# Kernel tuning notes

Hardware: AMD Instinct MI355X
Metric: run time of the kernel (lower is better)

Reference implementation:

```python
import jax, jax.numpy as jnp
import numpy as np

B, S, H, NH = 2, 2048, 128, 8  # batch, seq, num_hidden (= per-head dim), num_heads
LN_EPS = 1e-5


def _ln(x, g, b):
    m = jnp.mean(x, axis=-1, keepdims=True)
    v = jnp.var(x, axis=-1, keepdims=True)
    return (x - m) / jnp.sqrt(v + LN_EPS) * g + b


def setup_inputs() -> dict:
    key = jax.random.key(0)
    ks = jax.random.split(key, 18)
    sc = 0.02
    d = {}
    d["x"] = jax.random.normal(ks[0], (B, S, H), jnp.float32)
    # per-head full-dim projections, stacked over heads: [NH, H, H] (in->out layout)
    d["Wq"] = jax.random.normal(ks[1], (NH, H, H), jnp.float32) * sc
    d["bq"] = jax.random.normal(ks[2], (NH, H), jnp.float32) * sc
    d["Wk"] = jax.random.normal(ks[3], (NH, H, H), jnp.float32) * sc
    d["bk"] = jax.random.normal(ks[4], (NH, H), jnp.float32) * sc
    d["Wv"] = jax.random.normal(ks[5], (NH, H, H), jnp.float32) * sc
    d["bv"] = jax.random.normal(ks[6], (NH, H), jnp.float32) * sc
    d["Wo"] = jax.random.normal(ks[7], (NH * H, H), jnp.float32) * sc
    d["bo"] = jax.random.normal(ks[8], (H,), jnp.float32) * sc
    # conv1x1 FFN == pointwise linears: [H, 2H] and [2H, H]
    d["W1"] = jax.random.normal(ks[9], (H, 2 * H), jnp.float32) * sc
    d["b1"] = jax.random.normal(ks[10], (2 * H,), jnp.float32) * sc
    d["W2"] = jax.random.normal(ks[11], (2 * H, H), jnp.float32) * sc
    d["b2"] = jax.random.normal(ks[12], (H,), jnp.float32) * sc
    d["g1"] = jnp.ones((H,), jnp.float32)
    d["beta1"] = jnp.zeros((H,), jnp.float32)
    d["g2"] = jnp.ones((H,), jnp.float32)
    d["beta2"] = jnp.zeros((H,), jnp.float32)
    return d


def reference(x, Wq, bq, Wk, bk, Wv, bv, Wo, bo, W1, b1, W2, b2, g1, beta1, g2, beta2):
    # Multi-head attention: each head uses the FULL embed dim (faithful to source).
    Q = jnp.einsum('bsd,hde->bhse', x, Wq) + bq[None, :, None, :]
    K = jnp.einsum('bsd,hde->bhse', x, Wk) + bk[None, :, None, :]
    V = jnp.einsum('bsd,hde->bhse', x, Wv) + bv[None, :, None, :]
    scores = jnp.einsum('bhse,bhte->bhst', Q, K) / jnp.sqrt(jnp.float32(H))
    A = jax.nn.softmax(scores, axis=-1)          # [B, NH, S, S]
    o = jnp.einsum('bhst,bhte->bhse', A, V)      # [B, NH, S, H]
    o = o.transpose(0, 2, 1, 3).reshape(x.shape[0], x.shape[1], NH * H)  # concat heads
    y = o @ Wo + bo                               # W_O projection
    y = _ln(y, g1, beta1)                         # norm1 (no residual around attn, per source)
    f = jax.nn.relu(jax.nn.relu(y @ W1 + b1) @ W2 + b2)  # conv1x1 -> relu -> conv1x1 -> relu
    y = _ln(y + f, g2, beta2)                     # residual + norm2
    return y
```

## Files before the change

### kernel.cpp

```cpp
#include <hip/hip_runtime.h>
#include <math.h>

#define Bq  2
#define Sq  2048
#define Hq  128
#define NHq 8

typedef __attribute__((ext_vector_type(8))) short bf16x8;
typedef __attribute__((ext_vector_type(4))) float f32x4;
typedef __attribute__((ext_vector_type(16))) float f32x16;
typedef __attribute__((ext_vector_type(4))) unsigned short ushort4_t;
typedef __attribute__((ext_vector_type(4))) unsigned int uint4v;
typedef __attribute__((ext_vector_type(2))) unsigned long long u64x2;
typedef unsigned short ushort_t;
typedef unsigned int uint_t;
typedef unsigned long long u64;

__device__ inline ushort_t f2bf(float f) {
    union { float f; uint_t u; } c; c.f = f;
    uint_t u = c.u + 0x7FFFu + ((c.u >> 16) & 1u);
    return (ushort_t)(u >> 16);
}
__device__ inline float bf2f(ushort_t u) {
    union { uint_t u; float f; } c; c.u = ((uint_t)u) << 16;
    return c.f;
}

__device__ inline uint_t cvtpk_bf16(float lo, float hi) {
    uint_t r;
    asm("v_cvt_pk_bf16_f32 %0, %1, %2" : "=v"(r) : "v"(lo), "v"(hi));
    return r;
}
__device__ inline void pswap32(uint_t &a, uint_t &b) {
    asm("v_permlane32_swap_b32 %0, %1" : "+v"(a), "+v"(b));
}

#define GLOAD16(gsrc, ldst) \
    __builtin_amdgcn_global_load_lds( \
        (const __attribute__((address_space(1))) unsigned int*)(const void*)(gsrc), \
        (__attribute__((address_space(3))) unsigned int*)(ldst), 16, 0, 0)

__global__ __launch_bounds__(256) void tw_kernel(
    const float* __restrict__ Wq, const float* __restrict__ Wk, const float* __restrict__ Wv,
    const float* __restrict__ Wo, const float* __restrict__ W1, const float* __restrict__ W2,
    ushort_t* __restrict__ Wt_all, ushort_t* __restrict__ Wot,
    ushort_t* __restrict__ W1t, ushort_t* __restrict__ W2t)
{
    const int z = blockIdx.y;
    const float* src; ushort_t* dst; int R, C;
    if (z < 24) { const int h = z & 7;
        src = (z < 8 ? Wq : z < 16 ? Wk : Wv) + h * 16384;
        dst = Wt_all + z * 16384; R = 128; C = 128;
    } else if (z == 24) { src = Wo; dst = Wot; R = 1024; C = 128; }
    else if (z == 25)   { src = W1; dst = W1t; R = 128;  C = 256; }
    else                { src = W2; dst = W2t; R = 256;  C = 128; }

    const int tpc = C >> 5;
    if ((int)blockIdx.x >= (R >> 5) * tpc) return;
    const int r0 = (blockIdx.x / tpc) << 5;
    const int c0 = (blockIdx.x % tpc) << 5;

    __shared__ float ls[32][33];
    const int t = threadIdx.x;
    const int lr = t >> 5, lc = t & 31;
    #pragma unroll
    for (int i = 0; i < 4; ++i)
        ls[lr + i * 8][lc] = src[(size_t)(r0 + lr + i * 8) * C + c0 + lc];
    __syncthreads();
    const int wc = t >> 3, wr0 = (t & 7) << 2;
    ushort4_t o4;
    o4[0] = f2bf(ls[wr0 + 0][wc]); o4[1] = f2bf(ls[wr0 + 1][wc]);
    o4[2] = f2bf(ls[wr0 + 2][wc]); o4[3] = f2bf(ls[wr0 + 3][wc]);
    *(ushort4_t*)&dst[(size_t)(c0 + wc) * R + r0 + wr0] = o4;
}

__global__ __launch_bounds__(256) void qkv_gemm(
    const float* __restrict__ x, const ushort_t* __restrict__ Wt_all,
    const float* __restrict__ bq, const float* __restrict__ bk, const float* __restrict__ bv,
    ushort_t* __restrict__ Qb, ushort_t* __restrict__ Kb, ushort_t* __restrict__ Vb)
{
    __shared__ ushort_t As[64 * 128];
    __shared__ ushort_t Bs[128 * 128];
    const int tid = threadIdx.x;
    const int w = tid >> 6, l = tid & 63, lg = l >> 4, ln = l & 15;
    const int m0 = blockIdx.x << 6;
    const int z  = blockIdx.y;

    #pragma unroll
    for (int i = 0; i < 4; ++i) {
        const int c = tid + i * 256;
        const int row = c >> 4, j = c & 15;
        const float* xp = x + (size_t)(m0 + row) * 128 + j * 8;
        const float4 a = *(const float4*)xp;
        const float4 b = *(const float4*)(xp + 4);
        bf16x8 v;
        v[0]=f2bf(a.x); v[1]=f2bf(a.y); v[2]=f2bf(a.z); v[3]=f2bf(a.w);
        v[4]=f2bf(b.x); v[5]=f2bf(b.y); v[6]=f2bf(b.z); v[7]=f2bf(b.w);
        *(bf16x8*)&As[row * 128 + ((j ^ (row & 15)) << 3)] = v;
    }
    const ushort_t* Wz = Wt_all + (size_t)z * 16384;
    #pragma unroll
    for (int i = 0; i < 8; ++i) {
        const int seg = w * 8 + i;
        const int row = seg * 4 + (l >> 4);
        const int j = (l & 15) ^ (row & 15);
        GLOAD16(Wz + row * 128 + j * 8, &Bs[seg * 512]);
    }
    __syncthreads();

    bf16x8 af[4];
    #pragma unroll
    for (int kc = 0; kc < 4; ++kc)
        af[kc] = *(const bf16x8*)&As[(w * 16 + ln) * 128 + (((kc * 4 + lg) ^ ln) << 3)];

    f32x4 acc[8];
    #pragma unroll
    for (int nt = 0; nt < 8; ++nt) acc[nt] = (f32x4){0.f,0.f,0.f,0.f};
    #pragma unroll
    for (int nt = 0; nt < 8; ++nt)
        #pragma unroll
        for (int kc = 0; kc < 4; ++kc) {
            const bf16x8 bn = *(const bf16x8*)&Bs[(nt * 16 + ln) * 128 + (((kc * 4 + lg) ^ ln) << 3)];
            acc[nt] = __builtin_amdgcn_mfma_f32_16x16x32_bf16(af[kc], bn, acc[nt], 0, 0, 0);
        }

    const float* bias = (z < 8 ? bq : z < 16 ? bk : bv) + (z & 7) * 128;
    ushort_t* outp = (z < 8 ? Qb : z < 16 ? Kb : Vb);
    const float scale = z < 8 ? 0.08838834764831845f : 1.0f;
    const int h = z & 7;
    #pragma unroll
    for (int nt = 0; nt < 8; ++nt) {
        const float bb = bias[nt * 16 + ln];
        #pragma unroll
        for (int j2 = 0; j2 < 4; ++j2) {
            const int r = m0 + w * 16 + lg * 4 + j2;
            const int b = r >> 11, s = r & 2047;
            outp[((size_t)((b << 3) + h) * 2048 + s) * 128 + nt * 16 + ln] =
                f2bf((acc[nt][j2] + bb) * scale);
        }
    }
}

__global__ __launch_bounds__(256, 2) void attn_kernel(
    const ushort_t* __restrict__ Q, const ushort_t* __restrict__ K,
    const ushort_t* __restrict__ V, ushort_t* __restrict__ Opart,
    float2* __restrict__ ml)
{
    __shared__ ushort_t sh[32768];
    ushort_t* Vt = sh + 16384;

    const int tid = threadIdx.x;
    const int w = tid >> 6, l = tid & 63;
    const int ln5 = l & 31, h5 = l >> 5;

    const int id  = blockIdx.x;
    const int id2 = (id & 7) * 64 + (id >> 3);
    const int s   = id2 >> 8;
    const int bh  = (id2 >> 4) & 15;
    const int q0  = (id2 & 15) << 7;
    const int kv0 = s << 10;

    const size_t base = (size_t)bh * Sq * Hq;
    const ushort_t* Qp = Q + base;
    const ushort_t* Kp = K + base + (size_t)kv0 * Hq;
    const ushort_t* Vp = V + base + (size_t)kv0 * Hq;

    bf16x8 qf[8];
    {
        const ushort_t* qrow = Qp + (size_t)(q0 + w * 32 + ln5) * Hq;
        #pragma unroll
        for (int kc = 0; kc < 8; ++kc)
            qf[kc] = *(const bf16x8*)(qrow + kc * 16 + h5 * 8);
    }

    const int kv2 = (tid & 31) * 2;
    const int d8  = (tid >> 5) * 8;

    f32x16 po[4];
    #pragma unroll
    for (int dt = 0; dt < 4; ++dt)
        #pragma unroll
        for (int r = 0; r < 16; ++r) po[dt][r] = 0.f;
    float m_ = -1e30f, l_ = 0.f;

    #pragma unroll
    for (int i = 0; i < 4; ++i) {
        const int seg = w * 4 + i;
        const int row = seg * 4 + (l >> 4);
        const int j = (l & 15) ^ (row & 15);
        GLOAD16(Kp + (size_t)row * Hq + j * 8, &sh[seg * 512]);
    }
    bf16x8 va0 = *(const bf16x8*)(Vp + (size_t)kv2 * Hq + d8);
    bf16x8 va1 = *(const bf16x8*)(Vp + (size_t)(kv2 + 1) * Hq + d8);
    bf16x8 vb0 = *(const bf16x8*)(Vp + (size_t)kv2 * Hq + d8 + 64);
    bf16x8 vb1 = *(const bf16x8*)(Vp + (size_t)(kv2 + 1) * Hq + d8 + 64);
    __syncthreads();
    #pragma unroll
    for (int jj = 0; jj < 8; ++jj) {
        const int r1 = d8 + jj, r2 = d8 + 64 + jj;
        *(uint_t*)&Vt[r1 * 128 + ((((kv2 >> 3) ^ (r1 & 15))) << 3) + (kv2 & 7)] =
            (uint_t)(ushort_t)va0[jj] | ((uint_t)(ushort_t)va1[jj] << 16);
        *(uint_t*)&Vt[r2 * 128 + ((((kv2 >> 3) ^ (r2 & 15))) << 3) + (kv2 & 7)] =
            (uint_t)(ushort_t)vb0[jj] | ((uint_t)(ushort_t)vb1[jj] << 16);
    }
    __syncthreads();

    const int NT = 1024 / 64;
    for (int t = 0; t < NT; ++t) {
        const int buf = t & 1;
        const ushort_t* Ksb = sh + buf * 8192;

        f32x16 st[2];
        #pragma unroll
        for (int mt = 0; mt < 2; ++mt)
            #pragma unroll
            for (int r = 0; r < 16; ++r) st[mt][r] = 0.f;

        __builtin_amdgcn_s_setprio(1);
        #pragma unroll
        for (int kc = 0; kc < 8; ++kc) {
            #pragma unroll
            for (int mt = 0; mt < 2; ++mt) {
                const int row = mt * 32 + ln5;
                const int slot = (kc * 2 + h5) ^ (row & 15);
                const bf16x8 ka = *(const bf16x8*)&Ksb[row * 128 + (slot << 3)];
                st[mt] = __builtin_amdgcn_mfma_f32_32x32x16_bf16(ka, qf[kc], st[mt], 0, 0, 0);
            }
        }
        __builtin_amdgcn_s_setprio(0);

        if (t + 1 < NT) {
            const int k0n = (t + 1) * 64;
            #pragma unroll
            for (int i = 0; i < 4; ++i) {
                const int seg = w * 4 + i;
                const int row = seg * 4 + (l >> 4);
                const int j = (l & 15) ^ (row & 15);
                GLOAD16(Kp + (size_t)(k0n + row) * Hq + j * 8, &sh[(buf ^ 1) * 8192 + seg * 512]);
            }
            va0 = *(const bf16x8*)(Vp + (size_t)(k0n + kv2) * Hq + d8);
            va1 = *(const bf16x8*)(Vp + (size_t)(k0n + kv2 + 1) * Hq + d8);
            vb0 = *(const bf16x8*)(Vp + (size_t)(k0n + kv2) * Hq + d8 + 64);
            vb1 = *(const bf16x8*)(Vp + (size_t)(k0n + kv2 + 1) * Hq + d8 + 64);
        }

        float mxv[16];
        #pragma unroll
        for (int r = 0; r < 16; ++r) mxv[r] = fmaxf(st[0][r], st[1][r]);
        #pragma unroll
        for (int sd = 8; sd >= 1; sd >>= 1)
            #pragma unroll
            for (int i = 0; i < sd; ++i) mxv[i] = fmaxf(mxv[i], mxv[i + sd]);
        float mx = mxv[0];
        mx = fmaxf(mx, __shfl_xor(mx, 32));

        const bool anyup = __any(mx > m_ + 8.0f);
        float sc = 1.0f;
        if (anyup) {
            const float mn = fmaxf(m_, mx);
            sc = __expf(m_ - mn);
            m_ = mn;
        }

        float pe[32];
        #pragma unroll
        for (int mt = 0; mt < 2; ++mt)
            #pragma unroll
            for (int r = 0; r < 16; ++r)
                pe[mt * 16 + r] = __expf(st[mt][r] - m_);

        float sv[16];
        #pragma unroll
        for (int r = 0; r < 16; ++r) sv[r] = pe[r] + pe[16 + r];
        #pragma unroll
        for (int sd = 8; sd >= 1; sd >>= 1)
            #pragma unroll
            for (int i = 0; i < sd; ++i) sv[i] += sv[i + sd];
        float rs = sv[0];
        rs += __shfl_xor(rs, 32);
        l_ = l_ * sc + rs;

        bf16x8 pb[4];
        #pragma unroll
        for (int ks = 0; ks < 4; ++ks) {
            const int o = (ks >> 1) * 16 + (ks & 1) * 8;
            uint_t wA = cvtpk_bf16(pe[o + 0], pe[o + 1]);
            uint_t wB = cvtpk_bf16(pe[o + 4], pe[o + 5]);
            pswap32(wA, wB);
            uint_t wC = cvtpk_bf16(pe[o + 2], pe[o + 3]);
            uint_t wD = cvtpk_bf16(pe[o + 6], pe[o + 7]);
            pswap32(wC, wD);
            uint4v wv; wv[0] = wA; wv[1] = wC; wv[2] = wB; wv[3] = wD;
            pb[ks] = __builtin_bit_cast(bf16x8, wv);
        }

        if (anyup) {
            #pragma unroll
            for (int dt = 0; dt < 4; ++dt)
                #pragma unroll
                for (int r = 0; r < 16; ++r) po[dt][r] *= sc;
        }

        __builtin_amdgcn_s_setprio(1);
        #pragma unroll
        for (int dt = 0; dt < 4; ++dt) {
            #pragma unroll
            for (int ks = 0; ks < 4; ++ks) {
                const int row = dt * 32 + ln5;
                const int slot = (ks * 2 + h5) ^ (row & 15);
                const bf16x8 va = *(const bf16x8*)&Vt[row * 128 + (slot << 3)];
                po[dt] = __builtin_amdgcn_mfma_f32_32x32x16_bf16(va, pb[ks], po[dt], 0, 0, 0);
            }
        }
        __builtin_amdgcn_s_setprio(0);

        __syncthreads();
        if (t + 1 < NT) {
            #pragma unroll
            for (int jj = 0; jj < 8; ++jj) {
                const int r1 = d8 + jj, r2 = d8 + 64 + jj;
                *(uint_t*)&Vt[r1 * 128 + ((((kv2 >> 3) ^ (r1 & 15))) << 3) + (kv2 & 7)] =
                    (uint_t)(ushort_t)va0[jj] | ((uint_t)(ushort_t)va1[jj] << 16);
                *(uint_t*)&Vt[r2 * 128 + ((((kv2 >> 3) ^ (r2 & 15))) << 3) + (kv2 & 7)] =
                    (uint_t)(ushort_t)vb0[jj] | ((uint_t)(ushort_t)vb1[jj] << 16);
            }
        }
        __syncthreads();
    }

    char* shb = (char*)sh;
    char* wb = shb + w * 8448;
    #pragma unroll
    for (int dt = 0; dt < 4; ++dt)
        #pragma unroll
        for (int r = 0; r < 16; r += 2) {
            const int d = dt * 32 + (r & 3) + 8 * (r >> 2) + 4 * h5;
            const uint_t pk = cvtpk_bf16(po[dt][r], po[dt][r + 1]);
            *(uint_t*)(wb + ln5 * 264 + d * 2) = pk;
        }
    const int rid0 = (s * 16 + bh) * 2048 + q0 + w * 32;
    #pragma unroll
    for (int rb = 0; rb < 8; ++rb) {
        const int qr = rb * 4 + (l >> 4);
        const char* rp = wb + qr * 264 + (l & 15) * 16;
        u64x2 vv;
        vv[0] = *(const u64*)rp;
        vv[1] = *(const u64*)(rp + 8);
        *(u64x2*)(Opart + (size_t)(rid0 + qr) * 128 + (l & 15) * 8) = vv;
    }
    if (h5 == 0)
        ml[rid0 + ln5] = make_float2(m_, l_);
}

__global__ __launch_bounds__(256) void merge_kernel(
    const ushort_t* __restrict__ Opart, const float2* __restrict__ ml,
    ushort_t* __restrict__ ob)
{
    const int t = threadIdx.x;
    const int rid = blockIdx.x * 16 + (t >> 4);
    const int d0 = (t & 15) * 8;
    const float2 ml1 = ml[rid];
    const float2 ml2 = ml[32768 + rid];
    const float M = fmaxf(ml1.x, ml2.x);
    const float w1 = __expf(ml1.x - M), w2 = __expf(ml2.x - M);
    const float inv = 1.0f / (w1 * ml1.y + w2 * ml2.y);
    const bf16x8 o1 = *(const bf16x8*)&Opart[(size_t)rid * 128 + d0];
    const bf16x8 o2 = *(const bf16x8*)&Opart[(size_t)(32768 + rid) * 128 + d0];
    const int bh = rid >> 11, q = rid & 2047;
    const int b = bh >> 3, h = bh & 7;
    ushort_t* dst = ob + (size_t)(b * 2048 + q) * 1024 + h * 128 + d0;
    ushort4_t lo, hi;
    #pragma unroll
    for (int j = 0; j < 8; ++j) {
        const float v = (w1 * bf2f((ushort_t)o1[j]) + w2 * bf2f((ushort_t)o2[j])) * inv;
        if (j < 4) lo[j] = f2bf(v); else hi[j - 4] = f2bf(v);
    }
    *(ushort4_t*)dst = lo;
    *(ushort4_t*)(dst + 4) = hi;
}

__global__ __launch_bounds__(256) void gemm32_kernel(
    const ushort_t* __restrict__ A, const ushort_t* __restrict__ Bt,
    const float* __restrict__ bias, float* __restrict__ Cf, ushort_t* __restrict__ Cb,
    int N, int K, int KS, int relu)
{
    __shared__ ushort_t As[32 * 128];
    __shared__ ushort_t Bs[128 * 128];
    const int tid = threadIdx.x;
    const int w = tid >> 6, l = tid & 63, lg = l >> 4, ln = l & 15;
    const int m0 = blockIdx.x << 5;
    const int n0 = blockIdx.y << 7;
    const int rw = (w & 1) * 16;
    const int cw = (w >> 1) * 4;

    f32x4 acc[4];
    #pragma unroll
    for (int nt = 0; nt < 4; ++nt) acc[nt] = (f32x4){0.f,0.f,0.f,0.f};

    for (int ks = 0; ks < KS; ++ks) {
        const int k0 = ks << 7;
        #pragma unroll
        for (int i = 0; i < 2; ++i) {
            const int seg = w * 2 + i;
            const int row = seg * 4 + (l >> 4);
            const int j = (l & 15) ^ (row & 15);
            GLOAD16(A + (size_t)(m0 + row) * K + k0 + j * 8, &As[seg * 512]);
        }
        #pragma unroll
        for (int i = 0; i < 8; ++i) {
            const int seg = w * 8 + i;
            const int row = seg * 4 + (l >> 4);
            const int j = (l & 15) ^ (row & 15);
            GLOAD16(Bt + (size_t)(n0 + row) * K + k0 + j * 8, &Bs[seg * 512]);
        }
        __syncthreads();

        bf16x8 af[4];
        #pragma unroll
        for (int kc = 0; kc < 4; ++kc)
            af[kc] = *(const bf16x8*)&As[(rw + ln) * 128 + (((kc * 4 + lg) ^ ln) << 3)];
        #pragma unroll
        for (int nt = 0; nt < 4; ++nt)
            #pragma unroll
            for (int kc = 0; kc < 4; ++kc) {
                const bf16x8 bn = *(const bf16x8*)&Bs[((cw + nt) * 16 + ln) * 128 + (((kc * 4 + lg) ^ ln) << 3)];
                acc[nt] = __builtin_amdgcn_mfma_f32_16x16x32_bf16(af[kc], bn, acc[nt], 0, 0, 0);
            }
        __syncthreads();
    }

    #pragma unroll
    for (int nt = 0; nt < 4; ++nt) {
        const int col = n0 + (cw + nt) * 16 + ln;
        const float bb = bias[col];
        #pragma unroll
        for (int j2 = 0; j2 < 4; ++j2) {
            const int r = m0 + rw + lg * 4 + j2;
            float v = acc[nt][j2] + bb;
            if (relu) v = fmaxf(v, 0.f);
            if (Cb) Cb[(size_t)r * N + col] = f2bf(v);
            else    Cf[(size_t)r * N + col] = v;
        }
    }
}

__global__ __launch_bounds__(256) void ln_kernel(
    const float* __restrict__ in, const float* __restrict__ res,
    const float* __restrict__ g, const float* __restrict__ bta,
    float* __restrict__ out, ushort_t* __restrict__ out_bf)
{
    const int lane = threadIdx.x & 63;
    const int row  = (blockIdx.x << 2) + (threadIdx.x >> 6);
    const int base = row * 128 + lane * 2;
    float2 v = *(const float2*)&in[base];
    if (res) {
        const float2 rv = *(const float2*)&res[base];
        v.x += rv.x; v.y += rv.y;
    }
    float s  = v.x + v.y;
    float sq = v.x * v.x + v.y * v.y;
    #pragma unroll
    for (int mm = 1; mm <= 32; mm <<= 1) {
        s  += __shfl_xor(s, mm);
        sq += __shfl_xor(sq, mm);
    }
    const float mean = s * (1.0f / 128.0f);
    const float var  = sq * (1.0f / 128.0f) - mean * mean;
    const float rstd = rsqrtf(var + 1e-5f);
    const float2 gv = *(const float2*)&g[lane * 2];
    const float2 bv = *(const float2*)&bta[lane * 2];
    float2 o;
    o.x = (v.x - mean) * rstd * gv.x + bv.x;
    o.y = (v.y - mean) * rstd * gv.y + bv.y;
    *(float2*)&out[base] = o;
    if (out_bf) {
        const uint_t pk = (uint_t)f2bf(o.x) | ((uint_t)f2bf(o.y) << 16);
        *(uint_t*)&out_bf[base] = pk;
    }
}

extern "C" void kernel_launch(void* const* d_in, const int* in_sizes, int n_in,
                              void* d_out, int out_size, void* d_ws, size_t ws_size,
                              hipStream_t stream)
{
    const float* x   = (const float*)d_in[0];
    const float* Wq  = (const float*)d_in[1];
    const float* bq  = (const float*)d_in[2];
    const float* Wk  = (const float*)d_in[3];
    const float* bk  = (const float*)d_in[4];
    const float* Wv  = (const float*)d_in[5];
    const float* bv  = (const float*)d_in[6];
    const float* Wo  = (const float*)d_in[7];
    const float* bo  = (const float*)d_in[8];
    const float* W1  = (const float*)d_in[9];
    const float* b1  = (const float*)d_in[10];
    const float* W2  = (const float*)d_in[11];
    const float* b2  = (const float*)d_in[12];
    const float* g1  = (const float*)d_in[13];
    const float* be1 = (const float*)d_in[14];
    const float* g2  = (const float*)d_in[15];
    const float* be2 = (const float*)d_in[16];
    (void)in_sizes; (void)n_in; (void)out_size; (void)ws_size;

    ushort_t* Wt_all = (ushort_t*)d_ws;
    ushort_t* Wot = Wt_all + 393216;
    ushort_t* W1t = Wot + 131072;
    ushort_t* W2t = W1t + 32768;
    ushort_t* Qb  = W2t + 32768;
    ushort_t* Kb  = Qb + 4194304;
    ushort_t* Vb  = Kb + 4194304;
    ushort_t* ob  = Vb + 4194304;
    ushort_t* yb  = ob + 4194304;
    ushort_t* h1  = yb + 524288;
    ushort_t* Opart = h1 + 1048576;
    float2*   ml    = (float2*)(Opart + 8388608);
    float* y0 = (float*)Opart;
    float* y  = y0 + 524288;
    float* f  = y  + 524288;

    tw_kernel   <<<dim3(128, 27), 256, 0, stream>>>(Wq, Wk, Wv, Wo, W1, W2, Wt_all, Wot, W1t, W2t);
    qkv_gemm    <<<dim3(64, 24),  256, 0, stream>>>(x, Wt_all, bq, bk, bv, Qb, Kb, Vb);
    attn_kernel <<<dim3(512),     256, 0, stream>>>(Qb, Kb, Vb, Opart, ml);
    merge_kernel<<<dim3(2048),    256, 0, stream>>>(Opart, ml, ob);
    gemm32_kernel<<<dim3(128, 1), 256, 0, stream>>>(ob, Wot, bo, y0, nullptr, 128, 1024, 8, 0);
    ln_kernel   <<<1024,          256, 0, stream>>>(y0, nullptr, g1, be1, y, yb);
    gemm32_kernel<<<dim3(128, 2), 256, 0, stream>>>(yb, W1t, b1, nullptr, h1, 256, 128, 1, 1);
    gemm32_kernel<<<dim3(128, 1), 256, 0, stream>>>(h1, W2t, b2, f, nullptr, 128, 256, 2, 1);
    ln_kernel   <<<1024,          256, 0, stream>>>(y, f, g2, be2, (float*)d_out, nullptr);
}
```

Baseline: 95.87 us.

## Split attention KV four ways, fuse merge into Wo+LN, fuse FFN2 with LN

Attention now splits the KV range into four 512-key chunks, launching 1024 blocks. Its shared memory shrinks through a packed Vt layout, so three blocks can fit per CU. The separate merge kernel, Wo GEMM and first layernorm become one kernel that combines the four partials while staging A tiles. The second FFN GEMM is fused with residual-add and layernorm, and x is pre-converted to bf16 in the weight-transpose kernel so qkv_gemm can use async global-to-LDS loads. This cuts launches and intermediate global traffic, at the cost of more partial-output traffic and a serial 8-step K loop with only 128 blocks in the fused Wo kernel.

```diff
diff --git a/kernel.cpp b/kernel.cpp
--- a/kernel.cpp
+++ b/kernel.cpp
@@ -43,10 +43,30 @@
 __global__ __launch_bounds__(256) void tw_kernel(
     const float* __restrict__ Wq, const float* __restrict__ Wk, const float* __restrict__ Wv,
     const float* __restrict__ Wo, const float* __restrict__ W1, const float* __restrict__ W2,
+    const float* __restrict__ x,
     ushort_t* __restrict__ Wt_all, ushort_t* __restrict__ Wot,
-    ushort_t* __restrict__ W1t, ushort_t* __restrict__ W2t)
+    ushort_t* __restrict__ W1t, ushort_t* __restrict__ W2t, ushort_t* __restrict__ xb)
 {
     const int z = blockIdx.y;
+    const int t = threadIdx.x;
+
+    if (z == 27) {
+        const int r0 = blockIdx.x << 5;
+        #pragma unroll
+        for (int i = 0; i < 2; ++i) {
+            const int c = t + i * 256;
+            const int row = r0 + (c >> 4), j = (c & 15) * 8;
+            const float* xp = x + (size_t)row * 128 + j;
+            const float4 a = *(const float4*)xp;
+            const float4 b = *(const float4*)(xp + 4);
+            bf16x8 v;
+            v[0]=f2bf(a.x); v[1]=f2bf(a.y); v[2]=f2bf(a.z); v[3]=f2bf(a.w);
+            v[4]=f2bf(b.x); v[5]=f2bf(b.y); v[6]=f2bf(b.z); v[7]=f2bf(b.w);
+            *(bf16x8*)&xb[(size_t)row * 128 + j] = v;
+        }
+        return;
+    }
+
     const float* src; ushort_t* dst; int R, C;
     if (z < 24) { const int h = z & 7;
         src = (z < 8 ? Wq : z < 16 ? Wk : Wv) + h * 16384;
@@ -61,7 +81,6 @@
     const int c0 = (blockIdx.x % tpc) << 5;
 
     __shared__ float ls[32][33];
-    const int t = threadIdx.x;
     const int lr = t >> 5, lc = t & 31;
     #pragma unroll
     for (int i = 0; i < 4; ++i)
@@ -75,7 +94,7 @@
 }
 
 __global__ __launch_bounds__(256) void qkv_gemm(
-    const float* __restrict__ x, const ushort_t* __restrict__ Wt_all,
+    const ushort_t* __restrict__ xb, const ushort_t* __restrict__ Wt_all,
     const float* __restrict__ bq, const float* __restrict__ bk, const float* __restrict__ bv,
     ushort_t* __restrict__ Qb, ushort_t* __restrict__ Kb, ushort_t* __restrict__ Vb)
 {
@@ -88,15 +107,10 @@
 
     #pragma unroll
     for (int i = 0; i < 4; ++i) {
-        const int c = tid + i * 256;
-        const int row = c >> 4, j = c & 15;
-        const float* xp = x + (size_t)(m0 + row) * 128 + j * 8;
-        const float4 a = *(const float4*)xp;
-        const float4 b = *(const float4*)(xp + 4);
-        bf16x8 v;
-        v[0]=f2bf(a.x); v[1]=f2bf(a.y); v[2]=f2bf(a.z); v[3]=f2bf(a.w);
-        v[4]=f2bf(b.x); v[5]=f2bf(b.y); v[6]=f2bf(b.z); v[7]=f2bf(b.w);
-        *(bf16x8*)&As[row * 128 + ((j ^ (row & 15)) << 3)] = v;
+        const int seg = w * 4 + i;
+        const int row = seg * 4 + (l >> 4);
+        const int j = (l & 15) ^ (row & 15);
+        GLOAD16(xb + (size_t)(m0 + row) * 128 + j * 8, &As[seg * 512]);
     }
     const ushort_t* Wz = Wt_all + (size_t)z * 16384;
     #pragma unroll
@@ -141,12 +155,12 @@
     }
 }
 
-__global__ __launch_bounds__(256, 2) void attn_kernel(
+__global__ __launch_bounds__(256, 3) void attn_kernel(
     const ushort_t* __restrict__ Q, const ushort_t* __restrict__ K,
     const ushort_t* __restrict__ V, ushort_t* __restrict__ Opart,
     float2* __restrict__ ml)
 {
-    __shared__ ushort_t sh[32768];
+    __shared__ ushort_t sh[24576];
     ushort_t* Vt = sh + 16384;
 
     const int tid = threadIdx.x;
@@ -154,11 +168,11 @@
     const int ln5 = l & 31, h5 = l >> 5;
 
     const int id  = blockIdx.x;
-    const int id2 = (id & 7) * 64 + (id >> 3);
+    const int id2 = (id & 7) * 128 + (id >> 3);
     const int s   = id2 >> 8;
     const int bh  = (id2 >> 4) & 15;
     const int q0  = (id2 & 15) << 7;
-    const int kv0 = s << 10;
+    const int kv0 = s << 9;
 
     const size_t base = (size_t)bh * Sq * Hq;
     const ushort_t* Qp = Q + base;
@@ -182,6 +196,11 @@
         #pragma unroll
         for (int r = 0; r < 16; ++r) po[dt][r] = 0.f;
     float m_ = -1e30f, l_ = 0.f;
+
+    #define VT_WRITE(dd, pk) { \
+        const int R_ = (dd) >> 1; \
+        const int sp_ = (((dd) & 1) << 3) + (kv2 >> 3); \
+        *(uint_t*)&Vt[R_ * 128 + ((sp_ ^ (R_ & 15)) << 3) + (kv2 & 7)] = (pk); }
 
     #pragma unroll
     for (int i = 0; i < 4; ++i) {
@@ -197,15 +216,12 @@
     __syncthreads();
     #pragma unroll
     for (int jj = 0; jj < 8; ++jj) {
-        const int r1 = d8 + jj, r2 = d8 + 64 + jj;
-        *(uint_t*)&Vt[r1 * 128 + ((((kv2 >> 3) ^ (r1 & 15))) << 3) + (kv2 & 7)] =
-            (uint_t)(ushort_t)va0[jj] | ((uint_t)(ushort_t)va1[jj] << 16);
-        *(uint_t*)&Vt[r2 * 128 + ((((kv2 >> 3) ^ (r2 & 15))) << 3) + (kv2 & 7)] =
-            (uint_t)(ushort_t)vb0[jj] | ((uint_t)(ushort_t)vb1[jj] << 16);
+        VT_WRITE(d8 + jj,      (uint_t)(ushort_t)va0[jj] | ((uint_t)(ushort_t)va1[jj] << 16));
+        VT_WRITE(d8 + 64 + jj, (uint_t)(ushort_t)vb0[jj] | ((uint_t)(ushort_t)vb1[jj] << 16));
     }
     __syncthreads();
 
-    const int NT = 1024 / 64;
+    const int NT = 512 / 64;
     for (int t = 0; t < NT; ++t) {
         const int buf = t & 1;
         const ushort_t* Ksb = sh + buf * 8192;
@@ -306,9 +322,9 @@
         for (int dt = 0; dt < 4; ++dt) {
             #pragma unroll
             for (int ks = 0; ks < 4; ++ks) {
-                const int row = dt * 32 + ln5;
-                const int slot = (ks * 2 + h5) ^ (row & 15);
-                const bf16x8 va = *(const bf16x8*)&Vt[row * 128 + (slot << 3)];
+                const int R_ = dt * 16 + (ln5 >> 1);
+                const int sp_ = ((ln5 & 1) << 3) + ks * 2 + h5;
+                const bf16x8 va = *(const bf16x8*)&Vt[R_ * 128 + ((sp_ ^ (R_ & 15)) << 3)];
                 po[dt] = __builtin_amdgcn_mfma_f32_32x32x16_bf16(va, pb[ks], po[dt], 0, 0, 0);
             }
         }
@@ -318,18 +334,15 @@
         if (t + 1 < NT) {
             #pragma unroll
             for (int jj = 0; jj < 8; ++jj) {
-                const int r1 = d8 + jj, r2 = d8 + 64 + jj;
-                *(uint_t*)&Vt[r1 * 128 + ((((kv2 >> 3) ^ (r1 & 15))) << 3) + (kv2 & 7)] =
-                    (uint_t)(ushort_t)va0[jj] | ((uint_t)(ushort_t)va1[jj] << 16);
-                *(uint_t*)&Vt[r2 * 128 + ((((kv2 >> 3) ^ (r2 & 15))) << 3) + (kv2 & 7)] =
-                    (uint_t)(ushort_t)vb0[jj] | ((uint_t)(ushort_t)vb1[jj] << 16);
-            }
-        }
-        __syncthreads();
-    }
-
-    char* shb = (char*)sh;
-    char* wb = shb + w * 8448;
+                VT_WRITE(d8 + jj,      (uint_t)(ushort_t)va0[jj] | ((uint_t)(ushort_t)va1[jj] << 16));
+                VT_WRITE(d8 + 64 + jj, (uint_t)(ushort_t)vb0[jj] | ((uint_t)(ushort_t)vb1[jj] << 16));
+            }
+        }
+        __syncthreads();
+    }
+    #undef VT_WRITE
+
+    char* wb = (char*)sh + w * 8448;
     #pragma unroll
     for (int dt = 0; dt < 4; ++dt)
         #pragma unroll
@@ -352,37 +365,121 @@
         ml[rid0 + ln5] = make_float2(m_, l_);
 }
 
-__global__ __launch_bounds__(256) void merge_kernel(
+__global__ __launch_bounds__(256) void wo_ln_kernel(
     const ushort_t* __restrict__ Opart, const float2* __restrict__ ml,
-    ushort_t* __restrict__ ob)
+    const ushort_t* __restrict__ Wot, const float* __restrict__ bo,
+    const float* __restrict__ g1, const float* __restrict__ be1,
+    float* __restrict__ y, ushort_t* __restrict__ yb)
 {
-    const int t = threadIdx.x;
-    const int rid = blockIdx.x * 16 + (t >> 4);
-    const int d0 = (t & 15) * 8;
-    const float2 ml1 = ml[rid];
-    const float2 ml2 = ml[32768 + rid];
-    const float M = fmaxf(ml1.x, ml2.x);
-    const float w1 = __expf(ml1.x - M), w2 = __expf(ml2.x - M);
-    const float inv = 1.0f / (w1 * ml1.y + w2 * ml2.y);
-    const bf16x8 o1 = *(const bf16x8*)&Opart[(size_t)rid * 128 + d0];
-    const bf16x8 o2 = *(const bf16x8*)&Opart[(size_t)(32768 + rid) * 128 + d0];
-    const int bh = rid >> 11, q = rid & 2047;
-    const int b = bh >> 3, h = bh & 7;
-    ushort_t* dst = ob + (size_t)(b * 2048 + q) * 1024 + h * 128 + d0;
-    ushort4_t lo, hi;
-    #pragma unroll
-    for (int j = 0; j < 8; ++j) {
-        const float v = (w1 * bf2f((ushort_t)o1[j]) + w2 * bf2f((ushort_t)o2[j])) * inv;
-        if (j < 4) lo[j] = f2bf(v); else hi[j - 4] = f2bf(v);
-    }
-    *(ushort4_t*)dst = lo;
-    *(ushort4_t*)(dst + 4) = hi;
+    __shared__ ushort_t As[32 * 128];
+    __shared__ ushort_t Bs[128 * 128];
+    __shared__ float ybuf[32 * 132];
+    const int tid = threadIdx.x;
+    const int w = tid >> 6, l = tid & 63, lg = l >> 4, ln = l & 15;
+    const int m0 = blockIdx.x << 5;
+    const int rw = (w & 1) * 16;
+    const int cw = (w >> 1) * 4;
+
+    f32x4 acc[4];
+    #pragma unroll
+    for (int nt = 0; nt < 4; ++nt) acc[nt] = (f32x4){0.f,0.f,0.f,0.f};
+
+    for (int ks = 0; ks < 8; ++ks) {
+        const int k0 = ks << 7;
+        #pragma unroll
+        for (int i = 0; i < 2; ++i) {
+            const int c = tid + i * 256;
+            const int row = c >> 4, j = c & 15;
+            const int r = m0 + row, b = r >> 11, q = r & 2047;
+            const int prow = ((b << 3) + ks) * 2048 + q;
+            const float2 e0 = ml[prow];
+            const float2 e1 = ml[32768 + prow];
+            const float2 e2 = ml[65536 + prow];
+            const float2 e3 = ml[98304 + prow];
+            const float M = fmaxf(fmaxf(e0.x, e1.x), fmaxf(e2.x, e3.x));
+            const float w0 = __expf(e0.x - M), w1 = __expf(e1.x - M);
+            const float w2 = __expf(e2.x - M), w3 = __expf(e3.x - M);
+            const float inv = 1.0f / (w0 * e0.y + w1 * e1.y + w2 * e2.y + w3 * e3.y);
+            const size_t po_ = (size_t)prow * 128 + j * 8;
+            const bf16x8 o0 = *(const bf16x8*)&Opart[po_];
+            const bf16x8 o1 = *(const bf16x8*)&Opart[po_ + (size_t)32768 * 128];
+            const bf16x8 o2 = *(const bf16x8*)&Opart[po_ + (size_t)65536 * 128];
+            const bf16x8 o3 = *(const bf16x8*)&Opart[po_ + (size_t)98304 * 128];
+            bf16x8 mv;
+            #pragma unroll
+            for (int jj = 0; jj < 8; ++jj) {
+                const float v = (w0 * bf2f((ushort_t)o0[jj]) + w1 * bf2f((ushort_t)o1[jj]) +
+                                 w2 * bf2f((ushort_t)o2[jj]) + w3 * bf2f((ushort_t)o3[jj])) * inv;
+                mv[jj] = (short)f2bf(v);
+            }
+            *(bf16x8*)&As[row * 128 + ((j ^ (row & 15)) << 3)] = mv;
+        }
+        #pragma unroll
+        for (int i = 0; i < 8; ++i) {
+            const int seg = w * 8 + i;
+            const int row = seg * 4 + (l >> 4);
+            const int j = (l & 15) ^ (row & 15);
+            GLOAD16(Wot + (size_t)row * 1024 + k0 + j * 8, &Bs[seg * 512]);
+        }
+        __syncthreads();
+
+        bf16x8 af[4];
+        #pragma unroll
+        for (int kc = 0; kc < 4; ++kc)
+            af[kc] = *(const bf16x8*)&As[(rw + ln) * 128 + (((kc * 4 + lg) ^ ln) << 3)];
+        #pragma unroll
+        for (int nt = 0; nt < 4; ++nt)
+            #pragma unroll
+            for (int kc = 0; kc < 4; ++kc) {
+                const bf16x8 bn = *(const bf16x8*)&Bs[((cw + nt) * 16 + ln) * 128 + (((kc * 4 + lg) ^ ln) << 3)];
+                acc[nt] = __builtin_amdgcn_mfma_f32_16x16x32_bf16(af[kc], bn, acc[nt], 0, 0, 0);
+            }
+        __syncthreads();
+    }
+
+    #pragma unroll
+    for (int nt = 0; nt < 4; ++nt) {
+        const int col = (cw + nt) * 16 + ln;
+        const float bb = bo[col];
+        #pragma unroll
+        for (int j2 = 0; j2 < 4; ++j2)
+            ybuf[(rw + lg * 4 + j2) * 132 + col] = acc[nt][j2] + bb;
+    }
+    __syncthreads();
+
+    const int row = tid >> 3, sub = tid & 7;
+    float vals[16];
+    float sm = 0.f, sq = 0.f;
+    #pragma unroll
+    for (int e = 0; e < 16; ++e) {
+        const float v = ybuf[row * 132 + sub * 16 + e];
+        vals[e] = v; sm += v; sq += v * v;
+    }
+    #pragma unroll
+    for (int mmk = 1; mmk <= 4; mmk <<= 1) {
+        sm += __shfl_xor(sm, mmk);
+        sq += __shfl_xor(sq, mmk);
+    }
+    const float mean = sm * (1.0f / 128.0f);
+    const float var  = sq * (1.0f / 128.0f) - mean * mean;
+    const float rstd = rsqrtf(var + 1e-5f);
+    const int r = m0 + row;
+    float* yp = y + (size_t)r * 128 + sub * 16;
+    ushort_t* ybp = yb + (size_t)r * 128 + sub * 16;
+    #pragma unroll
+    for (int e = 0; e < 16; e += 2) {
+        const int col = sub * 16 + e;
+        const float v0 = (vals[e]   - mean) * rstd * g1[col]   + be1[col];
+        const float v1 = (vals[e+1] - mean) * rstd * g1[col+1] + be1[col+1];
+        yp[e] = v0; yp[e+1] = v1;
+        *(uint_t*)&ybp[e] = (uint_t)f2bf(v0) | ((uint_t)f2bf(v1) << 16);
+    }
 }
 
 __global__ __launch_bounds__(256) void gemm32_kernel(
     const ushort_t* __restrict__ A, const ushort_t* __restrict__ Bt,
-    const float* __restrict__ bias, float* __restrict__ Cf, ushort_t* __restrict__ Cb,
-    int N, int K, int KS, int relu)
+    const float* __restrict__ bias, ushort_t* __restrict__ Cb,
+    int N, int K, int KS)
 {
     __shared__ ushort_t As[32 * 128];
     __shared__ ushort_t Bs[128 * 128];
@@ -436,46 +533,96 @@
         #pragma unroll
         for (int j2 = 0; j2 < 4; ++j2) {
             const int r = m0 + rw + lg * 4 + j2;
-            float v = acc[nt][j2] + bb;
-            if (relu) v = fmaxf(v, 0.f);
-            if (Cb) Cb[(size_t)r * N + col] = f2bf(v);
-            else    Cf[(size_t)r * N + col] = v;
-        }
-    }
-}
-
-__global__ __launch_bounds__(256) void ln_kernel(
-    const float* __restrict__ in, const float* __restrict__ res,
-    const float* __restrict__ g, const float* __restrict__ bta,
-    float* __restrict__ out, ushort_t* __restrict__ out_bf)
+            Cb[(size_t)r * N + col] = f2bf(fmaxf(acc[nt][j2] + bb, 0.f));
+        }
+    }
+}
+
+__global__ __launch_bounds__(256) void ffn2_ln_kernel(
+    const ushort_t* __restrict__ h1, const ushort_t* __restrict__ W2t,
+    const float* __restrict__ b2, const float* __restrict__ y,
+    const float* __restrict__ g2, const float* __restrict__ be2,
+    float* __restrict__ out)
 {
-    const int lane = threadIdx.x & 63;
-    const int row  = (blockIdx.x << 2) + (threadIdx.x >> 6);
-    const int base = row * 128 + lane * 2;
-    float2 v = *(const float2*)&in[base];
-    if (res) {
-        const float2 rv = *(const float2*)&res[base];
-        v.x += rv.x; v.y += rv.y;
-    }
-    float s  = v.x + v.y;
-    float sq = v.x * v.x + v.y * v.y;
-    #pragma unroll
-    for (int mm = 1; mm <= 32; mm <<= 1) {
-        s  += __shfl_xor(s, mm);
-        sq += __shfl_xor(sq, mm);
-    }
-    const float mean = s * (1.0f / 128.0f);
+    __shared__ ushort_t As[32 * 128];
+    __shared__ ushort_t Bs[128 * 128];
+    __shared__ float ybuf[32 * 132];
+    const int tid = threadIdx.x;
+    const int w = tid >> 6, l = tid & 63, lg = l >> 4, ln = l & 15;
+    const int m0 = blockIdx.x << 5;
+    const int rw = (w & 1) * 16;
+    const int cw = (w >> 1) * 4;
+
+    f32x4 acc[4];
+    #pragma unroll
+    for (int nt = 0; nt < 4; ++nt) acc[nt] = (f32x4){0.f,0.f,0.f,0.f};
+
+    for (int ks = 0; ks < 2; ++ks) {
+        const int k0 = ks << 7;
+        #pragma unroll
+        for (int i = 0; i < 2; ++i) {
+            const int seg = w * 2 + i;
+            const int row = seg * 4 + (l >> 4);
+            const int j = (l & 15) ^ (row & 15);
+            GLOAD16(h1 + (size_t)(m0 + row) * 256 + k0 + j * 8, &As[seg * 512]);
+        }
+        #pragma unroll
+        for (int i = 0; i < 8; ++i) {
+            const int seg = w * 8 + i;
+            const int row = seg * 4 + (l >> 4);
+            const int j = (l & 15) ^ (row & 15);
+            GLOAD16(W2t + (size_t)row * 256 + k0 + j * 8, &Bs[seg * 512]);
+        }
+        __syncthreads();
+
+        bf16x8 af[4];
+        #pragma unroll
+        for (int kc = 0; kc < 4; ++kc)
+            af[kc] = *(const bf16x8*)&As[(rw + ln) * 128 + (((kc * 4 + lg) ^ ln) << 3)];
+        #pragma unroll
+        for (int nt = 0; nt < 4; ++nt)
+            #pragma unroll
+            for (int kc = 0; kc < 4; ++kc) {
+                const bf16x8 bn = *(const bf16x8*)&Bs[((cw + nt) * 16 + ln) * 128 + (((kc * 4 + lg) ^ ln) << 3)];
+                acc[nt] = __builtin_amdgcn_mfma_f32_16x16x32_bf16(af[kc], bn, acc[nt], 0, 0, 0);
+            }
+        __syncthreads();
+    }
+
+    #pragma unroll
+    for (int nt = 0; nt < 4; ++nt) {
+        const int col = (cw + nt) * 16 + ln;
+        const float bb = b2[col];
+        #pragma unroll
+        for (int j2 = 0; j2 < 4; ++j2) {
+            const int row = rw + lg * 4 + j2;
+            const float f = fmaxf(acc[nt][j2] + bb, 0.f);
+            ybuf[row * 132 + col] = f + y[(size_t)(m0 + row) * 128 + col];
+        }
+    }
+    __syncthreads();
+
+    const int row = tid >> 3, sub = tid & 7;
+    float vals[16];
+    float sm = 0.f, sq = 0.f;
+    #pragma unroll
+    for (int e = 0; e < 16; ++e) {
+        const float v = ybuf[row * 132 + sub * 16 + e];
+        vals[e] = v; sm += v; sq += v * v;
+    }
+    #pragma unroll
+    for (int mmk = 1; mmk <= 4; mmk <<= 1) {
+        sm += __shfl_xor(sm, mmk);
+        sq += __shfl_xor(sq, mmk);
+    }
+    const float mean = sm * (1.0f / 128.0f);
     const float var  = sq * (1.0f / 128.0f) - mean * mean;
     const float rstd = rsqrtf(var + 1e-5f);
-    const float2 gv = *(const float2*)&g[lane * 2];
-    const float2 bv = *(const float2*)&bta[lane * 2];
-    float2 o;
-    o.x = (v.x - mean) * rstd * gv.x + bv.x;
-    o.y = (v.y - mean) * rstd * gv.y + bv.y;
-    *(float2*)&out[base] = o;
-    if (out_bf) {
-        const uint_t pk = (uint_t)f2bf(o.x) | ((uint_t)f2bf(o.y) << 16);
-        *(uint_t*)&out_bf[base] = pk;
+    float* op = out + (size_t)(m0 + row) * 128 + sub * 16;
+    #pragma unroll
+    for (int e = 0; e < 16; ++e) {
+        const int col = sub * 16 + e;
+        op[e] = (vals[e] - mean) * rstd * g2[col] + be2[col];
     }
 }
 
@@ -503,28 +650,24 @@
     (void)in_sizes; (void)n_in; (void)out_size; (void)ws_size;
 
     ushort_t* Wt_all = (ushort_t*)d_ws;
-    ushort_t* Wot = Wt_all + 393216;
-    ushort_t* W1t = Wot + 131072;
-    ushort_t* W2t = W1t + 32768;
-    ushort_t* Qb  = W2t + 32768;
-    ushort_t* Kb  = Qb + 4194304;
-    ushort_t* Vb  = Kb + 4194304;
-    ushort_t* ob  = Vb + 4194304;
-    ushort_t* yb  = ob + 4194304;
-    ushort_t* h1  = yb + 524288;
-    ushort_t* Opart = h1 + 1048576;
-    float2*   ml    = (float2*)(Opart + 8388608);
-    float* y0 = (float*)Opart;
-    float* y  = y0 + 524288;
-    float* f  = y  + 524288;
-
-    tw_kernel   <<<dim3(128, 27), 256, 0, stream>>>(Wq, Wk, Wv, Wo, W1, W2, Wt_all, Wot, W1t, W2t);
-    qkv_gemm    <<<dim3(64, 24),  256, 0, stream>>>(x, Wt_all, bq, bk, bv, Qb, Kb, Vb);
-    attn_kernel <<<dim3(512),     256, 0, stream>>>(Qb, Kb, Vb, Opart, ml);
-    merge_kernel<<<dim3(2048),    256, 0, stream>>>(Opart, ml, ob);
-    gemm32_kernel<<<dim3(128, 1), 256, 0, stream>>>(ob, Wot, bo, y0, nullptr, 128, 1024, 8, 0);
-    ln_kernel   <<<1024,          256, 0, stream>>>(y0, nullptr, g1, be1, y, yb);
-    gemm32_kernel<<<dim3(128, 2), 256, 0, stream>>>(yb, W1t, b1, nullptr, h1, 256, 128, 1, 1);
-    gemm32_kernel<<<dim3(128, 1), 256, 0, stream>>>(h1, W2t, b2, f, nullptr, 128, 256, 2, 1);
-    ln_kernel   <<<1024,          256, 0, stream>>>(y, f, g2, be2, (float*)d_out, nullptr);
-}
+    ushort_t* Wot   = Wt_all + 393216;
+    ushort_t* W1t   = Wot + 131072;
+    ushort_t* W2t   = W1t + 32768;
+    ushort_t* xb    = W2t + 32768;
+    ushort_t* Qb    = xb + 524288;
+    ushort_t* Kb    = Qb + 4194304;
+    ushort_t* Vb    = Kb + 4194304;
+    ushort_t* Opart = Vb + 4194304;
+    float2*   ml    = (float2*)(Opart + 16777216);
+    float*    y  = (float*)Qb;
+    ushort_t* yb = Kb;
+    ushort_t* h1 = Opart;
+
+    tw_kernel    <<<dim3(128, 28), 256, 0, stream>>>(Wq, Wk, Wv, Wo, W1, W2, x,
+                                                     Wt_all, Wot, W1t, W2t, xb);
+    qkv_gemm     <<<dim3(64, 24),  256, 0, stream>>>(xb, Wt_all, bq, bk, bv, Qb, Kb, Vb);
+    attn_kernel  <<<dim3(1024),    256, 0, stream>>>(Qb, Kb, Vb, Opart, ml);
+    wo_ln_kernel <<<dim3(128),     256, 0, stream>>>(Opart, ml, Wot, bo, g1, be1, y, yb);
+    gemm32_kernel<<<dim3(128, 2),  256, 0, stream>>>(yb, W1t, b1, h1, 256, 128, 1);
+    ffn2_ln_kernel<<<dim3(128),    256, 0, stream>>>(h1, W2t, b2, y, g2, be2, (float*)d_out);
+}
```

Result: slower. 181.2 us (+89.0%).
